# Optimization experiments

Measured on AMD Instinct MI355X. Metric: run time of the kernel, lower is better.

## Reference

```python
import jax, jax.numpy as jnp
import numpy as np

EPS = 1e-5
B, C_IN, T_IN = 512, 12, 5000
NF, HID, LAT = 32, 64, 32


def setup_inputs() -> dict:
    key = jax.random.key(0)
    ks = jax.random.split(key, 12)
    inp = {
        "x": jax.random.normal(ks[0], (B, C_IN, T_IN), dtype=jnp.float32),
        # conv stack
        "conv1_w": jax.random.normal(ks[1], (32, C_IN, 50), dtype=jnp.float32) * 0.05,
        "conv1_b": jnp.zeros((32,), dtype=jnp.float32),
        "bn1_g": jnp.ones((32,), dtype=jnp.float32),
        "bn1_b": jnp.zeros((32,), dtype=jnp.float32),
        "conv2_w": jax.random.normal(ks[2], (NF, 32, 25), dtype=jnp.float32) * 0.05,
        "conv2_b": jnp.zeros((NF,), dtype=jnp.float32),
        "bn2_g": jnp.ones((NF,), dtype=jnp.float32),
        "bn2_b": jnp.zeros((NF,), dtype=jnp.float32),
        # input projection + layernorm
        "proj_w": jax.random.normal(ks[3], (LAT, NF), dtype=jnp.float32) * 0.1,
        "proj_b": jnp.zeros((LAT,), dtype=jnp.float32),
        "ln_g": jnp.ones((LAT,), dtype=jnp.float32),
        "ln_b": jnp.zeros((LAT,), dtype=jnp.float32),
        # PLRNN recurrence params
        "A": jnp.eye(LAT, dtype=jnp.float32) * 0.9,
        "W": jax.random.normal(ks[4], (LAT, HID), dtype=jnp.float32) * 0.1,
        "h_bias": jnp.zeros((HID,), dtype=jnp.float32),
        # output projection
        "out_w": jax.random.normal(ks[5], (LAT, LAT), dtype=jnp.float32) * 0.1,
        "out_b": jnp.zeros((LAT,), dtype=jnp.float32),
    }
    return inp


def _conv1d(x, w, b, stride):
    # x: [B, C, T], w: [O, I, K]
    y = jax.lax.conv_general_dilated(
        x, w, window_strides=(stride,), padding="VALID",
        dimension_numbers=("NCH", "OIH", "NCH"))
    return y + b[None, :, None]


def _batchnorm_train(x, g, b):
    # training-mode BN over (batch, time) per channel; x: [B, C, T]
    mean = jnp.mean(x, axis=(0, 2), keepdims=True)
    var = jnp.mean((x - mean) ** 2, axis=(0, 2), keepdims=True)
    return (x - mean) * jax.lax.rsqrt(var + EPS) * g[None, :, None] + b[None, :, None]


def _layernorm(x, g, b):
    mean = jnp.mean(x, axis=-1, keepdims=True)
    var = jnp.mean((x - mean) ** 2, axis=-1, keepdims=True)
    return (x - mean) * jax.lax.rsqrt(var + EPS) * g + b


def reference(x, conv1_w, conv1_b, bn1_g, bn1_b, conv2_w, conv2_b, bn2_g, bn2_b,
              proj_w, proj_b, ln_g, ln_b, A, W, h_bias, out_w, out_b):
    # conv front-end
    y = jax.nn.relu(_batchnorm_train(_conv1d(x, conv1_w, conv1_b, 10), bn1_g, bn1_b))
    y = jax.nn.relu(_batchnorm_train(_conv1d(y, conv2_w, conv2_b, 5), bn2_g, bn2_b))
    y = jnp.transpose(y, (0, 2, 1))  # [B, T, NF], T = 95

    # input projection + LN, vectorized over all timesteps
    xt = _layernorm(jnp.einsum("btf,lf->btl", y, proj_w) + proj_b, ln_g, ln_b)  # [B, T, L]
    xs = jnp.transpose(xt, (1, 0, 2))  # [T, B, L] for scan

    def step(h, x_t):
        # h: [B, L]
        linear = h @ A.T
        nonlinear = jax.nn.relu(h @ W + h_bias) @ W.T
        h_new = linear + nonlinear + x_t
        return h_new, h_new

    h0 = jnp.zeros((x.shape[0], A.shape[0]), dtype=x.dtype)
    _, outputs = jax.lax.scan(step, h0, xs)  # [T, B, L]

    pooled = jnp.mean(outputs, axis=0)  # [B, L]
    return pooled @ out_w.T + out_b
```

## Files before the change

kernel.cpp:

```cpp
#include <hip/hip_runtime.h>

#define NB    512
#define CIN   12
#define TIN   5000
#define C1    32
#define T1    496
#define T2    95
#define LATD  32
#define HIDD  64

#define OFS_STATS 0
#define OFS_W1P   256
#define OFS_W2P   19456
#define OFS_Y1    45056
#define OFS_Y2    8171520
#define OFS_XS    OFS_Y1

__global__ void prep_kernel(const float* __restrict__ w1, const float* __restrict__ w2,
                            float* __restrict__ ws) {
    int idx = blockIdx.x * 256 + threadIdx.x;
    if (idx < 256) ws[idx] = 0.f;
    int j = idx - 256;
    if (j >= 0 && j < 19200) {
        int ic = j / 1600, r = j % 1600;
        int p = r / 160, rr = r % 160, jj = rr / 32, oc = rr % 32;
        ws[OFS_W1P + j] = w1[oc * 600 + ic * 50 + 10 * jj + p];
    }
    int j2 = idx - 19456;
    if (j2 >= 0 && j2 < 25600) {
        int ic = j2 / 800, r = j2 % 800;
        int p = r / 160, rr = r % 160, jj = rr / 32, oc = rr % 32;
        ws[OFS_W2P + j2] = w2[oc * 800 + ic * 25 + 5 * jj + p];
    }
}

__global__ __launch_bounds__(256, 4) void conv1_kernel(const float* __restrict__ x,
                                                       const float* __restrict__ b1,
                                                       float* __restrict__ ws) {
    const float* w1p = ws + OFS_W1P;
    float* y1 = ws + OFS_Y1;
    float* stats = ws + OFS_STATS;
    int b  = blockIdx.x >> 1;
    int t0 = (blockIdx.x & 1) * 256;
    int tid = threadIdx.x;
    int ocg = tid & 7, tg = tid >> 3;
    int oc0 = ocg * 4, lt0 = tg * 8;

    __shared__ __align__(16) float xs_s[2][2680];
    __shared__ __align__(16) float ws_s[2][1600];
    __shared__ float sred[256];

    float acc[4][8];
#pragma unroll
    for (int a = 0; a < 4; ++a)
#pragma unroll
        for (int c = 0; c < 8; ++c) acc[a][c] = 0.f;

    const float* xb = x + (size_t)b * (CIN * TIN) + t0 * 10;
    int nvalid = TIN - t0 * 10;

    float4 px[3];
    float4 pw[2];

    auto fetch = [&](int ic) {
#pragma unroll
        for (int j = 0; j < 3; ++j) {
            int i = tid + j * 256;
            if (i < 650) {
                int src = 4 * i;
                const float* gp = xb + ic * TIN + src;
                float4 v;
                if (src + 4 <= nvalid) {
                    v = *(const float4*)gp;
                } else {
                    v.x = (src + 0 < nvalid) ? gp[0] : 0.f;
                    v.y = (src + 1 < nvalid) ? gp[1] : 0.f;
                    v.z = (src + 2 < nvalid) ? gp[2] : 0.f;
                    v.w = (src + 3 < nvalid) ? gp[3] : 0.f;
                }
                px[j] = v;
            }
        }
#pragma unroll
        for (int j = 0; j < 2; ++j) {
            int i = tid + j * 256;
            if (i < 400) pw[j] = *(const float4*)(w1p + ic * 1600 + 4 * i);
        }
    };

    auto stage = [&](int cur) {
#pragma unroll
        for (int j = 0; j < 3; ++j) {
            int i = tid + j * 256;
            if (i < 650) {
                int g = 4 * i;
                int col = g / 10, p = g - 10 * col;
                float vals[4] = {px[j].x, px[j].y, px[j].z, px[j].w};
#pragma unroll
                for (int m = 0; m < 4; ++m) {
                    int pm = p + m;
                    int rr = (pm >= 10) ? pm - 10 : pm;
                    int cc = col + ((pm >= 10) ? 1 : 0);
                    xs_s[cur][rr * 268 + cc] = vals[m];
                }
            }
        }
#pragma unroll
        for (int j = 0; j < 2; ++j) {
            int i = tid + j * 256;
            if (i < 400) *(float4*)&ws_s[cur][4 * i] = pw[j];
        }
    };

    fetch(0);
    stage(0);
    fetch(1);
    __syncthreads();

    for (int ic = 0; ic < CIN; ++ic) {
        int cur = ic & 1;
        if (ic + 1 < CIN) stage(cur ^ 1);
        if (ic + 2 < CIN) fetch(ic + 2);

#pragma unroll 2
        for (int p = 0; p < 10; ++p) {
            const float* xr = &xs_s[cur][p * 268 + 8 * tg];
            float4 xa = *(const float4*)(xr);
            float4 xbv = *(const float4*)(xr + 4);
            float4 xc = *(const float4*)(xr + 8);
            float xv[12] = {xa.x, xa.y, xa.z, xa.w,
                            xbv.x, xbv.y, xbv.z, xbv.w,
                            xc.x, xc.y, xc.z, xc.w};
            const float* wr = &ws_s[cur][p * 160 + oc0];
            float4 w0 = *(const float4*)(wr);
            float4 w1v = *(const float4*)(wr + 32);
            float4 w2v = *(const float4*)(wr + 64);
            float4 w3v = *(const float4*)(wr + 96);
            float4 w4v = *(const float4*)(wr + 128);
            float wj[5][4] = {{w0.x, w0.y, w0.z, w0.w},
                              {w1v.x, w1v.y, w1v.z, w1v.w},
                              {w2v.x, w2v.y, w2v.z, w2v.w},
                              {w3v.x, w3v.y, w3v.z, w3v.w},
                              {w4v.x, w4v.y, w4v.z, w4v.w}};
#pragma unroll
            for (int j = 0; j < 5; ++j)
#pragma unroll
                for (int jt = 0; jt < 8; ++jt) {
                    float xx = xv[jt + j];
#pragma unroll
                    for (int jo = 0; jo < 4; ++jo)
                        acc[jo][jt] = fmaf(wj[j][jo], xx, acc[jo][jt]);
                }
        }
        __syncthreads();
    }

    float bias[4];
#pragma unroll
    for (int jo = 0; jo < 4; ++jo) bias[jo] = b1[oc0 + jo];

    bool tvalid = (t0 + lt0) <= (T1 - 8);
    float psum[4], psq[4];
#pragma unroll
    for (int jo = 0; jo < 4; ++jo) {
        float s = 0.f, q = 0.f;
        if (tvalid) {
            float tmp[8];
#pragma unroll
            for (int jt = 0; jt < 8; ++jt) {
                float v = acc[jo][jt] + bias[jo];
                tmp[jt] = v; s += v; q = fmaf(v, v, q);
            }
            float* yrow = y1 + (size_t)(b * 32 + oc0 + jo) * T1 + t0 + lt0;
            float4 o0; o0.x = tmp[0]; o0.y = tmp[1]; o0.z = tmp[2]; o0.w = tmp[3];
            float4 o1; o1.x = tmp[4]; o1.y = tmp[5]; o1.z = tmp[6]; o1.w = tmp[7];
            *(float4*)yrow       = o0;
            *(float4*)(yrow + 4) = o1;
        }
        psum[jo] = s; psq[jo] = q;
    }
#pragma unroll
    for (int off = 32; off >= 8; off >>= 1) {
#pragma unroll
        for (int jo = 0; jo < 4; ++jo) {
            psum[jo] += __shfl_down(psum[jo], off, 64);
            psq[jo]  += __shfl_down(psq[jo],  off, 64);
        }
    }
    int lane = tid & 63, wvi = tid >> 6;
    if (lane < 8) {
#pragma unroll
        for (int jo = 0; jo < 4; ++jo) {
            sred[((wvi * 8 + lane) * 4 + jo) * 2 + 0] = psum[jo];
            sred[((wvi * 8 + lane) * 4 + jo) * 2 + 1] = psq[jo];
        }
    }
    __syncthreads();
    if (tid < 64) {
        int oc = tid >> 1, which = tid & 1;
        int og = oc >> 2, jo = oc & 3;
        float v = 0.f;
#pragma unroll
        for (int w = 0; w < 4; ++w)
            v += sred[((w * 8 + og) * 4 + jo) * 2 + which];
        atomicAdd(&stats[which * 32 + oc], v);
    }
}

__global__ __launch_bounds__(192, 2) void conv2_kernel(const float* __restrict__ b2,
                                                       const float* __restrict__ g1,
                                                       const float* __restrict__ be1,
                                                       float* __restrict__ ws) {
    const float* w2p = ws + OFS_W2P;
    const float* y1 = ws + OFS_Y1;
    float* y2 = ws + OFS_Y2;
    float* stats = ws + OFS_STATS;
    int b = blockIdx.x;
    int tid = threadIdx.x;
    int ocg = tid & 7, tg = tid >> 3;
    int oc0 = ocg * 4, lt0 = tg * 4;

    __shared__ __align__(16) float a1s[2][500];
    __shared__ __align__(16) float w2s[2][800];
    __shared__ float sred[192];
    __shared__ float bns[64];

    if (tid < 32) {
        float mean = stats[tid] * (1.f / 253952.f);
        float var  = stats[32 + tid] * (1.f / 253952.f) - mean * mean;
        float s = g1[tid] * rsqrtf(var + 1e-5f);
        bns[tid]      = s;
        bns[32 + tid] = be1[tid] - mean * s;
    }

    float acc[4][4];
#pragma unroll
    for (int a = 0; a < 4; ++a)
#pragma unroll
        for (int c = 0; c < 4; ++c) acc[a][c] = 0.f;

    float4 py, pw0, pw1;
    auto fetch = [&](int ic) {
        const float* yrow = y1 + (size_t)(b * 32 + ic) * T1;
        if (tid < 124) py = *(const float4*)(yrow + 4 * tid);
        pw0 = *(const float4*)(w2p + ic * 800 + 4 * tid);
        if (tid < 8) pw1 = *(const float4*)(w2p + ic * 800 + 4 * (tid + 192));
    };

    auto stage = [&](int ic, int cur) {
        if (tid < 124) {
            float s1 = bns[ic], sh1 = bns[32 + ic];
            float vals[4];
            vals[0] = fmaxf(fmaf(py.x, s1, sh1), 0.f);
            vals[1] = fmaxf(fmaf(py.y, s1, sh1), 0.f);
            vals[2] = fmaxf(fmaf(py.z, s1, sh1), 0.f);
            vals[3] = fmaxf(fmaf(py.w, s1, sh1), 0.f);
            int g = 4 * tid;
            int col = g / 5, p = g - 5 * col;
#pragma unroll
            for (int m = 0; m < 4; ++m) {
                int pm = p + m;
                int rr = (pm >= 5) ? pm - 5 : pm;
                int cc = col + ((pm >= 5) ? 1 : 0);
                a1s[cur][rr * 100 + cc] = vals[m];
            }
        }
        *(float4*)&w2s[cur][4 * tid] = pw0;
        if (tid < 8) *(float4*)&w2s[cur][4 * (tid + 192)] = pw1;
    };

    fetch(0);
    __syncthreads();
    stage(0, 0);
    fetch(1);
    __syncthreads();

    for (int ic = 0; ic < 32; ++ic) {
        int cur = ic & 1;
        if (ic + 1 < 32) stage(ic + 1, cur ^ 1);
        if (ic + 2 < 32) fetch(ic + 2);

#pragma unroll 2
        for (int p = 0; p < 5; ++p) {
            const float* xr = &a1s[cur][p * 100 + 4 * tg];
            float4 xa = *(const float4*)(xr);
            float4 xbv = *(const float4*)(xr + 4);
            float xv[8] = {xa.x, xa.y, xa.z, xa.w, xbv.x, xbv.y, xbv.z, xbv.w};
            const float* wr = &w2s[cur][p * 160 + oc0];
            float4 w0 = *(const float4*)(wr);
            float4 w1v = *(const float4*)(wr + 32);
            float4 w2v = *(const float4*)(wr + 64);
            float4 w3v = *(const float4*)(wr + 96);
            float4 w4v = *(const float4*)(wr + 128);
            float wj[5][4] = {{w0.x, w0.y, w0.z, w0.w},
                              {w1v.x, w1v.y, w1v.z, w1v.w},
                              {w2v.x, w2v.y, w2v.z, w2v.w},
                              {w3v.x, w3v.y, w3v.z, w3v.w},
                              {w4v.x, w4v.y, w4v.z, w4v.w}};
#pragma unroll
            for (int j = 0; j < 5; ++j)
#pragma unroll
                for (int jt = 0; jt < 4; ++jt) {
                    float xx = xv[jt + j];
#pragma unroll
                    for (int jo = 0; jo < 4; ++jo)
                        acc[jo][jt] = fmaf(wj[j][jo], xx, acc[jo][jt]);
                }
        }
        __syncthreads();
    }

    float bias[4];
#pragma unroll
    for (int jo = 0; jo < 4; ++jo) bias[jo] = b2[oc0 + jo];

    float psum[4], psq[4];
#pragma unroll
    for (int jo = 0; jo < 4; ++jo) {
        float s = 0.f, q = 0.f;
#pragma unroll
        for (int jt = 0; jt < 4; ++jt) {
            int t2 = lt0 + jt;
            if (t2 < T2) {
                float v = acc[jo][jt] + bias[jo];
                y2[(size_t)(b * 32 + oc0 + jo) * T2 + t2] = v;
                s += v; q = fmaf(v, v, q);
            }
        }
        psum[jo] = s; psq[jo] = q;
    }
#pragma unroll
    for (int off = 32; off >= 8; off >>= 1) {
#pragma unroll
        for (int jo = 0; jo < 4; ++jo) {
            psum[jo] += __shfl_down(psum[jo], off, 64);
            psq[jo]  += __shfl_down(psq[jo],  off, 64);
        }
    }
    int lane = tid & 63, wvi = tid >> 6;
    if (lane < 8) {
#pragma unroll
        for (int jo = 0; jo < 4; ++jo) {
            sred[((wvi * 8 + lane) * 4 + jo) * 2 + 0] = psum[jo];
            sred[((wvi * 8 + lane) * 4 + jo) * 2 + 1] = psq[jo];
        }
    }
    __syncthreads();
    if (tid < 64) {
        int oc = tid >> 1, which = tid & 1;
        int og = oc >> 2, jo = oc & 3;
        float v = 0.f;
#pragma unroll
        for (int w = 0; w < 3; ++w)
            v += sred[((w * 8 + og) * 4 + jo) * 2 + which];
        atomicAdd(&stats[64 + which * 32 + oc], v);
    }
}

__global__ __launch_bounds__(256, 2) void proj_kernel(const float* __restrict__ g2,
                                                      const float* __restrict__ be2,
                                                      const float* __restrict__ pw,
                                                      const float* __restrict__ pb,
                                                      const float* __restrict__ lng,
                                                      const float* __restrict__ lnb,
                                                      float* __restrict__ ws) {
    int b = blockIdx.x;
    int tid = threadIdx.x;
    __shared__ float a2s[3040];
    __shared__ float pws[1056];
    __shared__ float bns2[64];
    const float* stats = ws + OFS_STATS;
    const float* y2 = ws + OFS_Y2 + (size_t)b * (32 * T2);
    float* xsg = ws + OFS_XS;

    if (tid < 32) {
        float mean = stats[64 + tid] * (1.f / 48640.f);
        float var  = stats[96 + tid] * (1.f / 48640.f) - mean * mean;
        float s = g2[tid] * rsqrtf(var + 1e-5f);
        bns2[tid]      = s;
        bns2[32 + tid] = be2[tid] - mean * s;
    }
    __syncthreads();

    for (int f = 0; f < 32; ++f) {
        float s2  = bns2[f];
        float sh2 = bns2[32 + f];
        if (tid < T2)
            a2s[f * T2 + tid] = fmaxf(fmaf(y2[f * T2 + tid], s2, sh2), 0.f);
    }
    for (int i = tid; i < 1024; i += 256)
        pws[(i >> 5) * 33 + (i & 31)] = pw[i];

    int l = tid & 31, ts = tid >> 5;
    float pbv = pb[l], lg = lng[l], lb = lnb[l];
    __syncthreads();

    for (int it = 0; it < 12; ++it) {
        int t = ts + 8 * it;
        if (t < T2) {
            float v = pbv;
#pragma unroll
            for (int f = 0; f < 32; ++f)
                v = fmaf(a2s[f * T2 + t], pws[l * 33 + f], v);
            float sum = v;
#pragma unroll
            for (int off = 16; off >= 1; off >>= 1) sum += __shfl_xor(sum, off, 64);
            float mean = sum * (1.f / 32.f);
            float d = v - mean;
            float q = d * d;
#pragma unroll
            for (int off = 16; off >= 1; off >>= 1) q += __shfl_xor(q, off, 64);
            float o = d * rsqrtf(q * (1.f / 32.f) + 1e-5f) * lg + lb;
            xsg[(size_t)t * (NB * 32) + b * 32 + l] = o;
        }
    }
}

__global__ __launch_bounds__(64)
__attribute__((amdgpu_waves_per_eu(1, 1)))
void scan_kernel(const float* __restrict__ Am,
                 const float* __restrict__ Wm,
                 const float* __restrict__ hbp,
                 const float* __restrict__ ow,
                 const float* __restrict__ ob,
                 const float* __restrict__ ws,
                 float* __restrict__ out) {
    int b = blockIdx.x;
    int lane = threadIdx.x;
    int l = lane & 31, half = lane >> 5;
    __shared__ __align__(16) float hs[32];
    __shared__ __align__(16) float hds[64];
    __shared__ float ows[1056];

    float Wc[32], WT[32], Ah[16];
#pragma unroll
    for (int j = 0; j < 32; ++j) Wc[j] = Wm[j * HIDD + lane];
#pragma unroll
    for (int m = 0; m < 32; ++m) WT[m] = Wm[l * HIDD + half * 32 + m];
#pragma unroll
    for (int j = 0; j < 16; ++j) Ah[j] = Am[l * 32 + half * 16 + j];
    float hbv = hbp[lane];
    for (int i = lane; i < 1024; i += 64)
        ows[(i >> 5) * 33 + (i & 31)] = ow[i];

    const float* xsg = ws + OFS_XS + b * 32;
    if (lane < 32) hs[l] = 0.f;
    float xv = xsg[l];
    float pool = 0.f;
    __syncthreads();

    for (int t = 0; t < T2; ++t) {
        __syncthreads();
        float4 hv[8];
#pragma unroll
        for (int q = 0; q < 8; ++q) hv[q] = *(const float4*)&hs[4 * q];
        float a0 = hbv, a1 = 0.f, a2 = 0.f, a3 = 0.f;
#pragma unroll
        for (int q = 0; q < 8; ++q) {
            a0 = fmaf(Wc[4 * q + 0], hv[q].x, a0);
            a1 = fmaf(Wc[4 * q + 1], hv[q].y, a1);
            a2 = fmaf(Wc[4 * q + 2], hv[q].z, a2);
            a3 = fmaf(Wc[4 * q + 3], hv[q].w, a3);
        }
        float hid = fmaxf((a0 + a1) + (a2 + a3), 0.f);
        float4 hl[4];
#pragma unroll
        for (int q = 0; q < 4; ++q) hl[q] = *(const float4*)&hs[half * 16 + 4 * q];
        float l0 = 0.f, l1 = 0.f;
#pragma unroll
        for (int q = 0; q < 4; ++q) {
            l0 = fmaf(Ah[4 * q + 0], hl[q].x, l0);
            l1 = fmaf(Ah[4 * q + 1], hl[q].y, l1);
            l0 = fmaf(Ah[4 * q + 2], hl[q].z, l0);
            l1 = fmaf(Ah[4 * q + 3], hl[q].w, l1);
        }
        float lin = l0 + l1;
        hds[lane] = hid;
        __syncthreads();
        float n0 = 0.f, n1 = 0.f, n2 = 0.f, n3 = 0.f;
#pragma unroll
        for (int q = 0; q < 8; ++q) {
            float4 d4 = *(const float4*)&hds[half * 32 + 4 * q];
            n0 = fmaf(WT[4 * q + 0], d4.x, n0);
            n1 = fmaf(WT[4 * q + 1], d4.y, n1);
            n2 = fmaf(WT[4 * q + 2], d4.z, n2);
            n3 = fmaf(WT[4 * q + 3], d4.w, n3);
        }
        float part = (n0 + n1) + (n2 + n3) + lin;
        part += __shfl_xor(part, 32, 64);
        float hnew = part + xv;
        pool += hnew;
        if (t + 1 < T2) xv = xsg[(size_t)(t + 1) * (NB * 32) + l];
        if (lane < 32) hs[l] = hnew;
    }

    __syncthreads();
    if (lane < 32) hs[l] = pool * (1.f / 95.f);
    __syncthreads();
    if (lane < 32) {
        float4 p0 = *(const float4*)&hs[0];
        float4 p1 = *(const float4*)&hs[4];
        float4 p2 = *(const float4*)&hs[8];
        float4 p3 = *(const float4*)&hs[12];
        float4 p4 = *(const float4*)&hs[16];
        float4 p5 = *(const float4*)&hs[20];
        float4 p6 = *(const float4*)&hs[24];
        float4 p7 = *(const float4*)&hs[28];
        float o = ob[l];
        const float* owr = &ows[l * 33];
        o = fmaf(owr[0],  p0.x, o); o = fmaf(owr[1],  p0.y, o);
        o = fmaf(owr[2],  p0.z, o); o = fmaf(owr[3],  p0.w, o);
        o = fmaf(owr[4],  p1.x, o); o = fmaf(owr[5],  p1.y, o);
        o = fmaf(owr[6],  p1.z, o); o = fmaf(owr[7],  p1.w, o);
        o = fmaf(owr[8],  p2.x, o); o = fmaf(owr[9],  p2.y, o);
        o = fmaf(owr[10], p2.z, o); o = fmaf(owr[11], p2.w, o);
        o = fmaf(owr[12], p3.x, o); o = fmaf(owr[13], p3.y, o);
        o = fmaf(owr[14], p3.z, o); o = fmaf(owr[15], p3.w, o);
        o = fmaf(owr[16], p4.x, o); o = fmaf(owr[17], p4.y, o);
        o = fmaf(owr[18], p4.z, o); o = fmaf(owr[19], p4.w, o);
        o = fmaf(owr[20], p5.x, o); o = fmaf(owr[21], p5.y, o);
        o = fmaf(owr[22], p5.z, o); o = fmaf(owr[23], p5.w, o);
        o = fmaf(owr[24], p6.x, o); o = fmaf(owr[25], p6.y, o);
        o = fmaf(owr[26], p6.z, o); o = fmaf(owr[27], p6.w, o);
        o = fmaf(owr[28], p7.x, o); o = fmaf(owr[29], p7.y, o);
        o = fmaf(owr[30], p7.z, o); o = fmaf(owr[31], p7.w, o);
        out[b * 32 + l] = o;
    }
}

extern "C" void kernel_launch(void* const* d_in, const int* in_sizes, int n_in,
                              void* d_out, int out_size, void* d_ws, size_t ws_size,
                              hipStream_t stream) {
    (void)in_sizes; (void)n_in; (void)out_size; (void)ws_size;
    const float* x   = (const float*)d_in[0];
    const float* w1  = (const float*)d_in[1];
    const float* b1  = (const float*)d_in[2];
    const float* g1  = (const float*)d_in[3];
    const float* be1 = (const float*)d_in[4];
    const float* w2  = (const float*)d_in[5];
    const float* b2  = (const float*)d_in[6];
    const float* g2  = (const float*)d_in[7];
    const float* be2 = (const float*)d_in[8];
    const float* pw  = (const float*)d_in[9];
    const float* pb  = (const float*)d_in[10];
    const float* lng = (const float*)d_in[11];
    const float* lnb = (const float*)d_in[12];
    const float* Am  = (const float*)d_in[13];
    const float* Wm  = (const float*)d_in[14];
    const float* hb  = (const float*)d_in[15];
    const float* ow  = (const float*)d_in[16];
    const float* ob  = (const float*)d_in[17];
    float* ws  = (float*)d_ws;
    float* out = (float*)d_out;

    prep_kernel<<<176, 256, 0, stream>>>(w1, w2, ws);
    conv1_kernel<<<1024, 256, 0, stream>>>(x, b1, ws);
    conv2_kernel<<<512, 192, 0, stream>>>(b2, g1, be1, ws);
    proj_kernel<<<512, 256, 0, stream>>>(g2, be2, pw, pb, lng, lnb, ws);
    scan_kernel<<<512, 64, 0, stream>>>(Am, Wm, hb, ow, ob, ws, out);
}
```

Baseline: 409.8 us.

## Split conv2 input channels across two blocks with atomic accumulation

Conv2 now launches two blocks per batch element, each reducing over half of the input channels. The partial outputs are combined with atomicAdd into a y2 buffer that prep_kernel now zeroes first. Because no single block holds final y2 values anymore, BN2 statistics move into a new bnstats2 kernel that rereads y2. This doubles parallelism and raises the occupancy hint, at the cost of atomic traffic, a zeroing pass, an extra launch and an extra read of y2. The proj_kernel staging loop is also flattened to use all threads.

After: 448.8 us. 1.1x slower.

```diff
diff --git a/kernel.cpp b/kernel.cpp
--- a/kernel.cpp
+++ b/kernel.cpp
@@ -31,6 +31,11 @@
         int ic = j2 / 800, r = j2 % 800;
         int p = r / 160, rr = r % 160, jj = rr / 32, oc = rr % 32;
         ws[OFS_W2P + j2] = w2[oc * 800 + ic * 25 + 5 * jj + p];
+    }
+    int j3 = idx - 45056;
+    if (j3 >= 0 && j3 < 389120) {
+        float4 z; z.x = 0.f; z.y = 0.f; z.z = 0.f; z.w = 0.f;
+        *(float4*)&ws[OFS_Y2 + 4 * j3] = z;
     }
 }
 
@@ -207,7 +212,7 @@
     }
 }
 
-__global__ __launch_bounds__(192, 2) void conv2_kernel(const float* __restrict__ b2,
+__global__ __launch_bounds__(192, 3) void conv2_kernel(const float* __restrict__ b2,
                                                        const float* __restrict__ g1,
                                                        const float* __restrict__ be1,
                                                        float* __restrict__ ws) {
@@ -215,14 +220,15 @@
     const float* y1 = ws + OFS_Y1;
     float* y2 = ws + OFS_Y2;
     float* stats = ws + OFS_STATS;
-    int b = blockIdx.x;
+    int b = blockIdx.x >> 1;
+    int h = blockIdx.x & 1;
+    int icbase = 16 * h;
     int tid = threadIdx.x;
     int ocg = tid & 7, tg = tid >> 3;
     int oc0 = ocg * 4, lt0 = tg * 4;
 
     __shared__ __align__(16) float a1s[2][500];
     __shared__ __align__(16) float w2s[2][800];
-    __shared__ float sred[192];
     __shared__ float bns[64];
 
     if (tid < 32) {
@@ -269,16 +275,16 @@
         if (tid < 8) *(float4*)&w2s[cur][4 * (tid + 192)] = pw1;
     };
 
-    fetch(0);
-    __syncthreads();
-    stage(0, 0);
-    fetch(1);
-    __syncthreads();
-
-    for (int ic = 0; ic < 32; ++ic) {
-        int cur = ic & 1;
-        if (ic + 1 < 32) stage(ic + 1, cur ^ 1);
-        if (ic + 2 < 32) fetch(ic + 2);
+    fetch(icbase);
+    __syncthreads();
+    stage(icbase, 0);
+    fetch(icbase + 1);
+    __syncthreads();
+
+    for (int k = 0; k < 16; ++k) {
+        int cur = k & 1;
+        if (k + 1 < 16) stage(icbase + k + 1, cur ^ 1);
+        if (k + 2 < 16) fetch(icbase + k + 2);
 
 #pragma unroll 2
         for (int p = 0; p < 5; ++p) {
@@ -310,50 +316,43 @@
         __syncthreads();
     }
 
-    float bias[4];
-#pragma unroll
-    for (int jo = 0; jo < 4; ++jo) bias[jo] = b2[oc0 + jo];
-
-    float psum[4], psq[4];
 #pragma unroll
     for (int jo = 0; jo < 4; ++jo) {
-        float s = 0.f, q = 0.f;
+        float addb = (h == 0) ? b2[oc0 + jo] : 0.f;
 #pragma unroll
         for (int jt = 0; jt < 4; ++jt) {
             int t2 = lt0 + jt;
-            if (t2 < T2) {
-                float v = acc[jo][jt] + bias[jo];
-                y2[(size_t)(b * 32 + oc0 + jo) * T2 + t2] = v;
-                s += v; q = fmaf(v, v, q);
-            }
-        }
-        psum[jo] = s; psq[jo] = q;
-    }
-#pragma unroll
-    for (int off = 32; off >= 8; off >>= 1) {
-#pragma unroll
-        for (int jo = 0; jo < 4; ++jo) {
-            psum[jo] += __shfl_down(psum[jo], off, 64);
-            psq[jo]  += __shfl_down(psq[jo],  off, 64);
-        }
-    }
-    int lane = tid & 63, wvi = tid >> 6;
-    if (lane < 8) {
-#pragma unroll
-        for (int jo = 0; jo < 4; ++jo) {
-            sred[((wvi * 8 + lane) * 4 + jo) * 2 + 0] = psum[jo];
-            sred[((wvi * 8 + lane) * 4 + jo) * 2 + 1] = psq[jo];
-        }
-    }
-    __syncthreads();
-    if (tid < 64) {
-        int oc = tid >> 1, which = tid & 1;
-        int og = oc >> 2, jo = oc & 3;
-        float v = 0.f;
-#pragma unroll
-        for (int w = 0; w < 3; ++w)
-            v += sred[((w * 8 + og) * 4 + jo) * 2 + which];
-        atomicAdd(&stats[64 + which * 32 + oc], v);
+            if (t2 < T2)
+                atomicAdd(&y2[(size_t)(b * 32 + oc0 + jo) * T2 + t2],
+                          acc[jo][jt] + addb);
+        }
+    }
+}
+
+__global__ __launch_bounds__(256) void bnstats2_kernel(float* __restrict__ ws) {
+    const float* y2 = ws + OFS_Y2;
+    float* stats = ws + OFS_STATS;
+    int tid = threadIdx.x;
+    int oc = tid >> 3, slot = tid & 7;
+    int b0 = blockIdx.x * 4;
+    float s = 0.f, q = 0.f;
+#pragma unroll
+    for (int bb = 0; bb < 4; ++bb) {
+        const float* row = y2 + (size_t)((b0 + bb) * 32 + oc) * T2;
+#pragma unroll
+        for (int k = 0; k < 12; ++k) {
+            int t = slot + 8 * k;
+            if (t < T2) { float v = row[t]; s += v; q = fmaf(v, v, q); }
+        }
+    }
+#pragma unroll
+    for (int off = 1; off < 8; off <<= 1) {
+        s += __shfl_xor(s, off, 64);
+        q += __shfl_xor(q, off, 64);
+    }
+    if (slot == 0) {
+        atomicAdd(&stats[64 + oc], s);
+        atomicAdd(&stats[96 + oc], q);
     }
 }
 
@@ -382,11 +381,9 @@
     }
     __syncthreads();
 
-    for (int f = 0; f < 32; ++f) {
-        float s2  = bns2[f];
-        float sh2 = bns2[32 + f];
-        if (tid < T2)
-            a2s[f * T2 + tid] = fmaxf(fmaf(y2[f * T2 + tid], s2, sh2), 0.f);
+    for (int i = tid; i < 3040; i += 256) {
+        int f = i / 95;
+        a2s[i] = fmaxf(fmaf(y2[i], bns2[f], bns2[32 + f]), 0.f);
     }
     for (int i = tid; i < 1024; i += 256)
         pws[(i >> 5) * 33 + (i & 31)] = pw[i];
@@ -553,9 +550,10 @@
     float* ws  = (float*)d_ws;
     float* out = (float*)d_out;
 
-    prep_kernel<<<176, 256, 0, stream>>>(w1, w2, ws);
+    prep_kernel<<<1696, 256, 0, stream>>>(w1, w2, ws);
     conv1_kernel<<<1024, 256, 0, stream>>>(x, b1, ws);
-    conv2_kernel<<<512, 192, 0, stream>>>(b2, g1, be1, ws);
+    conv2_kernel<<<1024, 192, 0, stream>>>(b2, g1, be1, ws);
+    bnstats2_kernel<<<128, 256, 0, stream>>>(ws);
     proj_kernel<<<512, 256, 0, stream>>>(g2, be2, pw, pb, lng, lnb, ws);
     scan_kernel<<<512, 64, 0, stream>>>(Am, Wm, hb, ow, ob, ws, out);
 }
```
